# Kernel tuning notes

Hardware: AMD Instinct MI355X
Metric: run time of the kernel (lower is better)

The kernel has to match this reference:

```python
import jax, jax.numpy as jnp
import numpy as np

N_NODES = 50000
N_EDGES = 800000
IN_FEATS = 32
OUT_FEATS = 64
GRIDSIZE = 8


def setup_inputs() -> dict:
    key = jax.random.key(0)
    k1, k2, k3, k4 = jax.random.split(key, 4)
    x = jax.random.normal(k1, (N_NODES, IN_FEATS), dtype=jnp.float32)
    src = jax.random.randint(k2, (N_EDGES,), 0, N_NODES, dtype=jnp.int32)
    dst = jax.random.randint(k3, (N_EDGES,), 0, N_NODES, dtype=jnp.int32)
    scale = 1.0 / (np.sqrt(IN_FEATS) * np.sqrt(GRIDSIZE))
    fouriercoeffs = jax.random.normal(
        k4, (2, OUT_FEATS, IN_FEATS, GRIDSIZE), dtype=jnp.float32) * scale
    bias = jnp.zeros((OUT_FEATS,), dtype=jnp.float32)
    return {"x": x, "src": src, "dst": dst,
            "fouriercoeffs": fouriercoeffs, "bias": bias}


def reference(x, src, dst, fouriercoeffs, bias):
    # Per-edge source features: [E, in]
    src_feat = x[src]
    # Fourier frequencies k = 1..gridsize: [grid]
    k = jnp.arange(1, GRIDSIZE + 1, dtype=src_feat.dtype)
    # kx: [E, in, grid]
    kx = src_feat[:, :, None] * k[None, None, :]
    cos_kx = jnp.cos(kx)
    sin_kx = jnp.sin(kx)
    # Messages: einsum 'dbik,djik->bj' with d=2 stack of (cos, sin)
    m = (jnp.einsum('eik,jik->ej', cos_kx, fouriercoeffs[0])
         + jnp.einsum('eik,jik->ej', sin_kx, fouriercoeffs[1]))
    # Sum-scatter messages onto destination nodes: [N, out]
    h = jax.ops.segment_sum(m, dst, num_segments=N_NODES)
    return h + bias[None, :]
```

## Files before the change

### kernel.cpp

```cpp
#include <hip/hip_runtime.h>
#include <hip/hip_bf16.h>
#include <math.h>

#define IN_FEATS  32
#define OUT_FEATS 64
#define KDIM      512
#define NPB       32
#define ELLW      32
#define OVFCAP    4096

typedef __attribute__((ext_vector_type(8))) short bf16x8;
typedef __attribute__((ext_vector_type(4))) float f32x4;

static __device__ __forceinline__ unsigned short f2bf(float f) {
    unsigned u = __builtin_bit_cast(unsigned, f);
    return (unsigned short)((u + 0x7fffu + ((u >> 16) & 1u)) >> 16);
}
static __device__ __forceinline__ float bf2f(unsigned short h) {
    return __builtin_bit_cast(float, (unsigned)h << 16);
}

__global__ __launch_bounds__(256) void fkan_nmf(
    const float* __restrict__ x,
    const float* __restrict__ fc,
    const int* __restrict__ src,
    const int* __restrict__ dst,
    unsigned short* __restrict__ M,
    int* __restrict__ cnt,
    unsigned short* __restrict__ ebuf,
    int* __restrict__ ovf_cnt,
    int2* __restrict__ ovf,
    int n_nodes, int n_edges, int node_blocks, int fill_blocks)
{
    __shared__ __align__(16) short phi[NPB * KDIM];
    const int b   = blockIdx.x;
    const int tid = threadIdx.x;

    if (b & 1) {
        const int f = b >> 1;
        if (f >= fill_blocks) return;
        const int e0 = (f * 256 + tid) * 2;
        if (e0 >= n_edges) return;
        if (e0 + 1 < n_edges) {
            const int2 d2 = *(const int2*)(dst + e0);
            const int2 s2 = *(const int2*)(src + e0);
            {
                const int pos = atomicAdd(&cnt[d2.x], 1);
                if (pos < ELLW) {
                    ebuf[(size_t)d2.x * ELLW + pos] = (unsigned short)s2.x;
                } else {
                    const int op = atomicAdd(ovf_cnt, 1);
                    if (op < OVFCAP) { ovf[op].x = d2.x; ovf[op].y = s2.x; }
                }
            }
            {
                const int pos = atomicAdd(&cnt[d2.y], 1);
                if (pos < ELLW) {
                    ebuf[(size_t)d2.y * ELLW + pos] = (unsigned short)s2.y;
                } else {
                    const int op = atomicAdd(ovf_cnt, 1);
                    if (op < OVFCAP) { ovf[op].x = d2.y; ovf[op].y = s2.y; }
                }
            }
        } else {
            const int d = dst[e0];
            const int s = src[e0];
            const int pos = atomicAdd(&cnt[d], 1);
            if (pos < ELLW) {
                ebuf[(size_t)d * ELLW + pos] = (unsigned short)s;
            } else {
                const int op = atomicAdd(ovf_cnt, 1);
                if (op < OVFCAP) { ovf[op].x = d; ovf[op].y = s; }
            }
        }
        return;
    }

    const int nbt = b >> 1;
    if (nbt >= node_blocks) return;
    const int lane  = tid & 63;
    const int wid   = tid >> 6;
    const int nbase = nbt * NPB;

    const int j0   = wid * 16;
    const int brow = j0 + (lane & 15);
    const int kofs = 8 * (lane >> 4);
    bf16x8 bfrag[16];
#pragma unroll
    for (int ks = 0; ks < 16; ++ks) {
        const int K  = ks * 32 + kofs;
        const int br = K >> 8;
        const int ik = K & 255;
        const float* p = fc + ((size_t)(br * OUT_FEATS + brow) * 256 + ik);
        const float4 f0 = *(const float4*)p;
        const float4 f1 = *(const float4*)(p + 4);
        bf16x8 t;
        t[0] = (short)f2bf(f0.x); t[1] = (short)f2bf(f0.y);
        t[2] = (short)f2bf(f0.z); t[3] = (short)f2bf(f0.w);
        t[4] = (short)f2bf(f1.x); t[5] = (short)f2bf(f1.y);
        t[6] = (short)f2bf(f1.z); t[7] = (short)f2bf(f1.w);
        bfrag[ks] = t;
    }

    {
        const int node = tid >> 3;
        const int q    = tid & 7;
        const int n    = nbase + node;
        char* rowp = (char*)phi + node * 1024;
        const int sw = (node & 7) << 4;
        float xv[4];
        if (n < n_nodes) {
            const float4 a = *(const float4*)(x + (size_t)n * 32 + q * 4);
            xv[0] = a.x; xv[1] = a.y; xv[2] = a.z; xv[3] = a.w;
        } else {
#pragma unroll
            for (int u = 0; u < 4; ++u) xv[u] = 0.f;
        }
#pragma unroll
        for (int u = 0; u < 4; ++u) {
            const int i = q * 4 + u;
            const float f  = xv[u] * 0.15915494309189535f;
            const float fr = f - floorf(f);
            const float s1 = __builtin_amdgcn_sinf(fr);
            const float c1 = __builtin_amdgcn_cosf(fr);
            const float twoc = 2.f * c1;
            float cAm = 1.f, sAm = 0.f, cA = c1, sA = s1;
            int pcv[4], psv[4];
#pragma unroll
            for (int p = 0; p < 4; ++p) {
                const float cB = twoc * cA - cAm;
                const float sB = twoc * sA - sAm;
                pcv[p] = (int)(((unsigned)f2bf(cB) << 16) | f2bf(cA));
                psv[p] = (int)(((unsigned)f2bf(sB) << 16) | f2bf(sA));
                const float cN = twoc * cB - cA;
                const float sN = twoc * sB - sA;
                cAm = cB; sAm = sB; cA = cN; sA = sN;
            }
            int4 vc; vc.x = pcv[0]; vc.y = pcv[1]; vc.z = pcv[2]; vc.w = pcv[3];
            int4 vs; vs.x = psv[0]; vs.y = psv[1]; vs.z = psv[2]; vs.w = psv[3];
            *(int4*)(rowp + ((i * 16) ^ sw))       = vc;
            *(int4*)(rowp + ((512 + i * 16) ^ sw)) = vs;
        }
    }
    __syncthreads();

    f32x4 acc[2] = {{0.f,0.f,0.f,0.f},{0.f,0.f,0.f,0.f}};
    const int arow = lane & 15;
    const int sw   = (arow & 7) << 4;
    const int kbyt = 16 * (lane >> 4);
#pragma unroll
    for (int ks = 0; ks < 16; ++ks) {
#pragma unroll
        for (int nt = 0; nt < 2; ++nt) {
            const int row = nt * 16 + arow;
            const bf16x8 afrag = *(const bf16x8*)
                ((const char*)phi + row * 1024 + ((ks * 64 + kbyt) ^ sw));
            acc[nt] = __builtin_amdgcn_mfma_f32_16x16x32_bf16(
                afrag, bfrag[ks], acc[nt], 0, 0, 0);
        }
    }

    const int rem = n_nodes - nbase;
#pragma unroll
    for (int nt = 0; nt < 2; ++nt) {
        const int rbase = nt * 16 + (lane >> 4) * 4;
#pragma unroll
        for (int r = 0; r < 4; ++r) {
            const int node = rbase + r;
            if (node < rem)
                M[(size_t)(nbase + node) * OUT_FEATS + j0 + (lane & 15)] =
                    f2bf(acc[nt][r]);
        }
    }
}

__global__ __launch_bounds__(256) void fkan_gather(
    const int* __restrict__ cnt, const unsigned short* __restrict__ ebuf,
    const unsigned short* __restrict__ M, const float* __restrict__ bias,
    float* __restrict__ out, int n_nodes)
{
    const int tid  = threadIdx.x;
    const int lane = tid & 63;
    const int node = blockIdx.x * 8 + (tid >> 6) * 2 + (lane >> 5);
    if (node >= n_nodes) return;
    const int len = min(cnt[node], ELLW);
    const unsigned short* row = ebuf + (size_t)node * ELLW;
    const int l32  = lane & 31;
    const int sub  = l32 >> 3;
    const int colb = (l32 & 7) * 8;
    float acc[8] = {0.f,0.f,0.f,0.f,0.f,0.f,0.f,0.f};
    const bf16x8 vz = {0,0,0,0,0,0,0,0};
    const unsigned ones = 0x3F803F80u;
    for (int e = 0; e < len; e += 8) {
        const int eeA = e + sub;
        const int eeB = e + 4 + sub;
        const bool pA = eeA < len;
        const bool pB = eeB < len;
        const int sA = pA ? row[eeA] : 0;
        const int sB = pB ? row[eeB] : 0;
        const bf16x8 vA = pA ? *(const bf16x8*)(M + (size_t)sA * OUT_FEATS + colb) : vz;
        const bf16x8 vB = pB ? *(const bf16x8*)(M + (size_t)sB * OUT_FEATS + colb) : vz;
        const uint4 ua = __builtin_bit_cast(uint4, vA);
        const uint4 ub = __builtin_bit_cast(uint4, vB);
        const unsigned uaw[4] = {ua.x, ua.y, ua.z, ua.w};
        const unsigned ubw[4] = {ub.x, ub.y, ub.z, ub.w};
#pragma unroll
        for (int w = 0; w < 4; ++w) {
            const unsigned lo = __builtin_amdgcn_perm(uaw[w], ubw[w], 0x05040100u);
            const unsigned hi = __builtin_amdgcn_perm(uaw[w], ubw[w], 0x07060302u);
            asm("v_dot2_f32_bf16 %0, %1, %2, %0"
                : "+v"(acc[2 * w]) : "v"(lo), "v"(ones));
            asm("v_dot2_f32_bf16 %0, %1, %2, %0"
                : "+v"(acc[2 * w + 1]) : "v"(hi), "v"(ones));
        }
    }
#pragma unroll
    for (int m = 8; m <= 16; m <<= 1) {
#pragma unroll
        for (int c = 0; c < 8; ++c) acc[c] += __shfl_xor(acc[c], m);
    }
    if (sub == 0) {
        const float4 b0 = *(const float4*)(bias + colb);
        const float4 b1 = *(const float4*)(bias + colb + 4);
        float4 o0; o0.x = acc[0] + b0.x; o0.y = acc[1] + b0.y;
                   o0.z = acc[2] + b0.z; o0.w = acc[3] + b0.w;
        float4 o1; o1.x = acc[4] + b1.x; o1.y = acc[5] + b1.y;
                   o1.z = acc[6] + b1.z; o1.w = acc[7] + b1.w;
        *(float4*)(out + (size_t)node * OUT_FEATS + colb)     = o0;
        *(float4*)(out + (size_t)node * OUT_FEATS + colb + 4) = o1;
    }
}

__global__ __launch_bounds__(256) void fkan_ovf(
    const int* __restrict__ ovf_cnt, const int2* __restrict__ ovf,
    const unsigned short* __restrict__ M, float* __restrict__ out)
{
    const int total = min(ovf_cnt[0], OVFCAP) * 16;
    for (int t = blockIdx.x * 256 + threadIdx.x; t < total; t += gridDim.x * 256) {
        const int e = t >> 4;
        const int q = t & 15;
        const int d = ovf[e].x;
        const int s = ovf[e].y;
        const unsigned short* mp = M + (size_t)s * OUT_FEATS + q * 4;
        float* op = out + (size_t)d * OUT_FEATS + q * 4;
        atomicAdd(op + 0, bf2f(mp[0]));
        atomicAdd(op + 1, bf2f(mp[1]));
        atomicAdd(op + 2, bf2f(mp[2]));
        atomicAdd(op + 3, bf2f(mp[3]));
    }
}

extern "C" void kernel_launch(void* const* d_in, const int* in_sizes, int n_in,
                              void* d_out, int out_size, void* d_ws, size_t ws_size,
                              hipStream_t stream)
{
    const float* x    = (const float*)d_in[0];
    const int*   src  = (const int*)d_in[1];
    const int*   dst  = (const int*)d_in[2];
    const float* fc   = (const float*)d_in[3];
    const float* bias = (const float*)d_in[4];
    float* out = (float*)d_out;

    const int n_nodes = in_sizes[0] / IN_FEATS;
    const int n_edges = in_sizes[1];

    const int node_blocks = (n_nodes + NPB - 1) / NPB;
    const int fill_blocks = (n_edges + 511) / 512;
    const int m = max(node_blocks, fill_blocks);
    const int total_blocks = 2 * m;

    char* ws = (char*)d_ws;
    unsigned short* M    = (unsigned short*)ws;
    unsigned short* ebuf = (unsigned short*)(ws + (size_t)n_nodes * OUT_FEATS * 2);
    int* cnt     = (int*)((char*)ebuf + (size_t)n_nodes * ELLW * 2);
    int* ovf_cnt = cnt + n_nodes;
    int2* ovf    = (int2*)(ovf_cnt + 1);

    hipMemsetAsync(cnt, 0, ((size_t)n_nodes + 1) * sizeof(int), stream);

    fkan_nmf<<<total_blocks, 256, 0, stream>>>(
        x, fc, src, dst, M, cnt, ebuf, ovf_cnt, ovf,
        n_nodes, n_edges, node_blocks, fill_blocks);

    fkan_gather<<<(n_nodes + 7) / 8, 256, 0, stream>>>(
        cnt, ebuf, M, bias, out, n_nodes);

    fkan_ovf<<<16, 256, 0, stream>>>(ovf_cnt, ovf, M, out);
}
```

Measured before the change: 85.39 us.

## Split fused node/fill kernel, fold counter reset into node kernel, double nodes per block

Separates the interleaved node-message and edge-fill blocks into two kernels. The counter zeroing moves into the node-message kernel, which removes the memset launch. Nodes per block rise from 32 to 64, so each block amortizes the B-fragment load over more MFMA work, at the cost of twice the shared memory and fewer resident blocks. Splitting the kernels gives up the overlap between the fill atomics and the matrix compute that the fused kernel allowed.

```diff
diff --git a/kernel.cpp b/kernel.cpp
--- a/kernel.cpp
+++ b/kernel.cpp
@@ -5,7 +5,7 @@
 #define IN_FEATS  32
 #define OUT_FEATS 64
 #define KDIM      512
-#define NPB       32
+#define NPB       64
 #define ELLW      32
 #define OVFCAP    4096
 
@@ -20,67 +20,25 @@
     return __builtin_bit_cast(float, (unsigned)h << 16);
 }
 
-__global__ __launch_bounds__(256) void fkan_nmf(
+__global__ __launch_bounds__(256) void fkan_node_msg(
     const float* __restrict__ x,
     const float* __restrict__ fc,
-    const int* __restrict__ src,
-    const int* __restrict__ dst,
     unsigned short* __restrict__ M,
     int* __restrict__ cnt,
-    unsigned short* __restrict__ ebuf,
     int* __restrict__ ovf_cnt,
-    int2* __restrict__ ovf,
-    int n_nodes, int n_edges, int node_blocks, int fill_blocks)
+    int n_nodes)
 {
     __shared__ __align__(16) short phi[NPB * KDIM];
-    const int b   = blockIdx.x;
-    const int tid = threadIdx.x;
-
-    if (b & 1) {
-        const int f = b >> 1;
-        if (f >= fill_blocks) return;
-        const int e0 = (f * 256 + tid) * 2;
-        if (e0 >= n_edges) return;
-        if (e0 + 1 < n_edges) {
-            const int2 d2 = *(const int2*)(dst + e0);
-            const int2 s2 = *(const int2*)(src + e0);
-            {
-                const int pos = atomicAdd(&cnt[d2.x], 1);
-                if (pos < ELLW) {
-                    ebuf[(size_t)d2.x * ELLW + pos] = (unsigned short)s2.x;
-                } else {
-                    const int op = atomicAdd(ovf_cnt, 1);
-                    if (op < OVFCAP) { ovf[op].x = d2.x; ovf[op].y = s2.x; }
-                }
-            }
-            {
-                const int pos = atomicAdd(&cnt[d2.y], 1);
-                if (pos < ELLW) {
-                    ebuf[(size_t)d2.y * ELLW + pos] = (unsigned short)s2.y;
-                } else {
-                    const int op = atomicAdd(ovf_cnt, 1);
-                    if (op < OVFCAP) { ovf[op].x = d2.y; ovf[op].y = s2.y; }
-                }
-            }
-        } else {
-            const int d = dst[e0];
-            const int s = src[e0];
-            const int pos = atomicAdd(&cnt[d], 1);
-            if (pos < ELLW) {
-                ebuf[(size_t)d * ELLW + pos] = (unsigned short)s;
-            } else {
-                const int op = atomicAdd(ovf_cnt, 1);
-                if (op < OVFCAP) { ovf[op].x = d; ovf[op].y = s; }
-            }
-        }
-        return;
-    }
-
-    const int nbt = b >> 1;
-    if (nbt >= node_blocks) return;
-    const int lane  = tid & 63;
-    const int wid   = tid >> 6;
-    const int nbase = nbt * NPB;
+    const int tid  = threadIdx.x;
+    const int lane = tid & 63;
+    const int wid  = tid >> 6;
+    const int nbase = blockIdx.x * NPB;
+
+    if (tid < NPB) {
+        const int n = nbase + tid;
+        if (n < n_nodes) cnt[n] = 0;
+    }
+    if (blockIdx.x == 0 && tid == NPB) ovf_cnt[0] = 0;
 
     const int j0   = wid * 16;
     const int brow = j0 + (lane & 15);
@@ -103,22 +61,24 @@
     }
 
     {
-        const int node = tid >> 3;
-        const int q    = tid & 7;
+        const int node = tid >> 2;
+        const int q    = tid & 3;
         const int n    = nbase + node;
         char* rowp = (char*)phi + node * 1024;
         const int sw = (node & 7) << 4;
-        float xv[4];
+        float xv[8];
         if (n < n_nodes) {
-            const float4 a = *(const float4*)(x + (size_t)n * 32 + q * 4);
-            xv[0] = a.x; xv[1] = a.y; xv[2] = a.z; xv[3] = a.w;
+            const float4 a = *(const float4*)(x + (size_t)n * 32 + q * 8);
+            const float4 b = *(const float4*)(x + (size_t)n * 32 + q * 8 + 4);
+            xv[0]=a.x; xv[1]=a.y; xv[2]=a.z; xv[3]=a.w;
+            xv[4]=b.x; xv[5]=b.y; xv[6]=b.z; xv[7]=b.w;
         } else {
 #pragma unroll
-            for (int u = 0; u < 4; ++u) xv[u] = 0.f;
-        }
-#pragma unroll
-        for (int u = 0; u < 4; ++u) {
-            const int i = q * 4 + u;
+            for (int u = 0; u < 8; ++u) xv[u] = 0.f;
+        }
+#pragma unroll
+        for (int u = 0; u < 8; ++u) {
+            const int i = q * 8 + u;
             const float f  = xv[u] * 0.15915494309189535f;
             const float fr = f - floorf(f);
             const float s1 = __builtin_amdgcn_sinf(fr);
@@ -144,14 +104,15 @@
     }
     __syncthreads();
 
-    f32x4 acc[2] = {{0.f,0.f,0.f,0.f},{0.f,0.f,0.f,0.f}};
+    f32x4 acc[4] = {{0.f,0.f,0.f,0.f},{0.f,0.f,0.f,0.f},
+                    {0.f,0.f,0.f,0.f},{0.f,0.f,0.f,0.f}};
     const int arow = lane & 15;
     const int sw   = (arow & 7) << 4;
     const int kbyt = 16 * (lane >> 4);
 #pragma unroll
     for (int ks = 0; ks < 16; ++ks) {
 #pragma unroll
-        for (int nt = 0; nt < 2; ++nt) {
+        for (int nt = 0; nt < 4; ++nt) {
             const int row = nt * 16 + arow;
             const bf16x8 afrag = *(const bf16x8*)
                 ((const char*)phi + row * 1024 + ((ks * 64 + kbyt) ^ sw));
@@ -162,7 +123,7 @@
 
     const int rem = n_nodes - nbase;
 #pragma unroll
-    for (int nt = 0; nt < 2; ++nt) {
+    for (int nt = 0; nt < 4; ++nt) {
         const int rbase = nt * 16 + (lane >> 4) * 4;
 #pragma unroll
         for (int r = 0; r < 4; ++r) {
@@ -170,6 +131,47 @@
             if (node < rem)
                 M[(size_t)(nbase + node) * OUT_FEATS + j0 + (lane & 15)] =
                     f2bf(acc[nt][r]);
+        }
+    }
+}
+
+__global__ __launch_bounds__(256) void fkan_fill(
+    const int* __restrict__ src, const int* __restrict__ dst,
+    int* __restrict__ cnt, unsigned short* __restrict__ ebuf,
+    int* __restrict__ ovf_cnt, int2* __restrict__ ovf, int n_edges)
+{
+    const int e0 = (blockIdx.x * 256 + threadIdx.x) * 2;
+    if (e0 >= n_edges) return;
+    if (e0 + 1 < n_edges) {
+        const int2 d2 = *(const int2*)(dst + e0);
+        const int2 s2 = *(const int2*)(src + e0);
+        {
+            const int pos = atomicAdd(&cnt[d2.x], 1);
+            if (pos < ELLW) {
+                ebuf[(size_t)d2.x * ELLW + pos] = (unsigned short)s2.x;
+            } else {
+                const int op = atomicAdd(ovf_cnt, 1);
+                if (op < OVFCAP) { ovf[op].x = d2.x; ovf[op].y = s2.x; }
+            }
+        }
+        {
+            const int pos = atomicAdd(&cnt[d2.y], 1);
+            if (pos < ELLW) {
+                ebuf[(size_t)d2.y * ELLW + pos] = (unsigned short)s2.y;
+            } else {
+                const int op = atomicAdd(ovf_cnt, 1);
+                if (op < OVFCAP) { ovf[op].x = d2.y; ovf[op].y = s2.y; }
+            }
+        }
+    } else {
+        const int d = dst[e0];
+        const int s = src[e0];
+        const int pos = atomicAdd(&cnt[d], 1);
+        if (pos < ELLW) {
+            ebuf[(size_t)d * ELLW + pos] = (unsigned short)s;
+        } else {
+            const int op = atomicAdd(ovf_cnt, 1);
+            if (op < OVFCAP) { ovf[op].x = d; ovf[op].y = s; }
         }
     }
 }
@@ -264,11 +266,6 @@
     const int n_nodes = in_sizes[0] / IN_FEATS;
     const int n_edges = in_sizes[1];
 
-    const int node_blocks = (n_nodes + NPB - 1) / NPB;
-    const int fill_blocks = (n_edges + 511) / 512;
-    const int m = max(node_blocks, fill_blocks);
-    const int total_blocks = 2 * m;
-
     char* ws = (char*)d_ws;
     unsigned short* M    = (unsigned short*)ws;
     unsigned short* ebuf = (unsigned short*)(ws + (size_t)n_nodes * OUT_FEATS * 2);
@@ -276,11 +273,11 @@
     int* ovf_cnt = cnt + n_nodes;
     int2* ovf    = (int2*)(ovf_cnt + 1);
 
-    hipMemsetAsync(cnt, 0, ((size_t)n_nodes + 1) * sizeof(int), stream);
-
-    fkan_nmf<<<total_blocks, 256, 0, stream>>>(
-        x, fc, src, dst, M, cnt, ebuf, ovf_cnt, ovf,
-        n_nodes, n_edges, node_blocks, fill_blocks);
+    fkan_node_msg<<<(n_nodes + NPB - 1) / NPB, 256, 0, stream>>>(
+        x, fc, M, cnt, ovf_cnt, n_nodes);
+
+    fkan_fill<<<(n_edges + 511) / 512, 256, 0, stream>>>(
+        src, dst, cnt, ebuf, ovf_cnt, ovf, n_edges);
 
     fkan_gather<<<(n_nodes + 7) / 8, 256, 0, stream>>>(
         cnt, ebuf, M, bias, out, n_nodes);
```

Result: slower. 96.65 us (+13.2%).
